# Performance work log

Measured on AMD Instinct MI355X. Metric: run time of the kernel, lower is better.

The kernel has to match this reference:

```python
import jax, jax.numpy as jnp
import numpy as np

B, N, IN, H, K, D, L = 8, 1024, 32, 32, 3, 16, 2  # batch, nodes, input_dim, hidden, cheb_k, embed_dim, layers


def setup_inputs() -> dict:
    key = jax.random.key(0)
    ks = jax.random.split(key, 4 + 4 * L)
    inp = {
        "xt": jax.random.normal(ks[0], (B, N, IN), jnp.float32),
        "init_state": jax.random.normal(ks[1], (L, B, N, H), jnp.float32),
        # row-normalized-ish support so the Chebyshev recursion stays bounded
        "support": jax.random.uniform(ks[2], (N, N), jnp.float32) / N,
        "embeddings": jax.random.normal(ks[3], (B, N, D), jnp.float32),
    }
    i = 4
    for l in range(L):
        cin = IN if l == 0 else H
        gi = K * (cin + H)
        inp[f"gate_w{l}"] = jax.random.normal(ks[i], (D, gi, 2 * H), jnp.float32) * (2.0 / (gi + 2 * H)) ** 0.5; i += 1
        inp[f"gate_b{l}"] = jax.random.normal(ks[i], (D, 2 * H), jnp.float32) * 0.05; i += 1
        inp[f"upd_w{l}"] = jax.random.normal(ks[i], (D, gi, H), jnp.float32) * (2.0 / (gi + H)) ** 0.5; i += 1
        inp[f"upd_b{l}"] = jax.random.normal(ks[i], (D, H), jnp.float32) * 0.05; i += 1
    return inp


def _cheb_gconv(x, support, emb, w_pool, b_pool):
    """HimGCN_share forward, meta_axis='ST', 2-D support.
    x: [B,N,C]; support: [N,N]; emb: [B,N,D];
    w_pool: [D, K*C, O]; b_pool: [D, O]. Returns [B,N,O]."""
    n = support.shape[0]
    graphs = [jnp.eye(n, dtype=x.dtype), support]
    for _ in range(2, K):
        graphs.append(2.0 * support @ graphs[-1] - graphs[-2])
    G = jnp.stack(graphs)                                   # [K,N,N]
    c = x.shape[-1]
    x_g = jnp.einsum('knm,bmc->bnkc', G, x).reshape(x.shape[0], n, K * c)  # concat over k
    # faithful to einsum('bni,bnio->bno') with bnio = einsum('bnd,dio->bnio'),
    # contracted in a memory-lighter order (same math)
    xe = jnp.einsum('bni,bnd->bnid', x_g, emb)              # [B,N,K*C,D]
    out = jnp.einsum('bnid,dio->bno', xe, w_pool)
    out = out + jnp.einsum('bnd,do->bno', emb, b_pool)
    return out


def _gcru_cell(x, state, support, emb, gw, gb, uw, ub):
    inp = jnp.concatenate([x, state], axis=-1)
    z_r = jax.nn.sigmoid(_cheb_gconv(inp, support, emb, gw, gb))
    z, r = z_r[..., :H], z_r[..., H:]
    cand = jnp.concatenate([x, z * state], axis=-1)
    hc = jnp.tanh(_cheb_gconv(cand, support, emb, uw, ub))
    return r * state + (1.0 - r) * hc


def reference(xt, init_state, support, embeddings,
              gate_w0, gate_b0, upd_w0, upd_b0,
              gate_w1, gate_b1, upd_w1, upd_b1):
    params = [(gate_w0, gate_b0, upd_w0, upd_b0), (gate_w1, gate_b1, upd_w1, upd_b1)]
    cur = xt
    hidden = []
    for l in range(L):
        gw, gb, uw, ub = params[l]
        cur = _gcru_cell(cur, init_state[l], support, embeddings, gw, gb, uw, ub)
        hidden.append(cur)
    return cur, jnp.stack(hidden)
```

## Files before the change

### kernel.cpp

```cpp
#include <hip/hip_runtime.h>
#include <math.h>

#define BB 8
#define NN 1024
#define HH 32
#define II 192
#define DD 16
#define BN (BB*NN)
#define FR 512

typedef __attribute__((ext_vector_type(8))) short short8v;
typedef __attribute__((ext_vector_type(4))) float float4v;

union Frag8 { short8v v; uint2 u[2]; uint4 q; };

static __device__ inline ushort bf(float x) {
  union { float f; unsigned u; } c; c.f = x;
  unsigned r = c.u + 0x7FFFu + ((c.u >> 16) & 1u);
  return (ushort)(r >> 16);
}

static __device__ inline uint4 pack8(const ushort e[8]) {
  uint4 v;
  v.x = (unsigned)e[0] | ((unsigned)e[1] << 16);
  v.y = (unsigned)e[2] | ((unsigned)e[3] << 16);
  v.z = (unsigned)e[4] | ((unsigned)e[5] << 16);
  v.w = (unsigned)e[6] | ((unsigned)e[7] << 16);
  return v;
}

template <int O>
static __device__ void prep_w_frag(const float* __restrict__ W,
                                   ushort* __restrict__ WF, int d,
                                   float* lds)
{
  constexpr int NCG = O / 16;
  const float* Wd = W + (size_t)d * II * O;
  ushort* WFd = WF + (size_t)d * NCG * 6 * FR;
  const int tid = threadIdx.x;
  for (int f = tid; f < II * O / 4; f += 256) {
    int i = f / (O / 4);
    int o4 = (f % (O / 4)) * 4;
    float4 v = *(const float4*)(Wd + (size_t)i * O + o4);
    lds[i * (O + 1) + o4 + 0] = v.x; lds[i * (O + 1) + o4 + 1] = v.y;
    lds[i * (O + 1) + o4 + 2] = v.z; lds[i * (O + 1) + o4 + 3] = v.w;
  }
  __syncthreads();
  for (int f = tid; f < NCG * 6 * 64; f += 256) {
    int rem = f % 384;
    int ks = rem >> 6, l = rem & 63;
    int o = (f / 384) * 16 + (l & 15);
    int kb = ks * 32 + (l >> 4) * 4;
    ushort e[8];
#pragma unroll
    for (int j = 0; j < 4; ++j) {
      e[j] = bf(lds[(kb + j) * (O + 1) + o]);
      e[4 + j] = bf(lds[(kb + 16 + j) * (O + 1) + o]);
    }
    *(uint4*)(WFd + (size_t)f * 8) = pack8(e);
  }
}

__global__ __launch_bounds__(256) void prep_all(
    const float* __restrict__ S,
    ushort* __restrict__ SbF, ushort* __restrict__ S2bF,
    const float* __restrict__ gw0, const float* __restrict__ gw1,
    ushort* __restrict__ wfg0, ushort* __restrict__ wfg1,
    const float* __restrict__ uw0, const float* __restrict__ uw1,
    ushort* __restrict__ wfu0, ushort* __restrict__ wfu1,
    const float* __restrict__ xt, const float* __restrict__ st0,
    const float* __restrict__ st1,
    ushort* __restrict__ xbTFg0, ushort* __restrict__ xbTFg1)
{
  union PrepSm {
    float wlds[II * 65];
    struct { ushort A[32][136]; ushort Bt[32][132]; ushort C2[32][36]; } s2;
    ushort T[32 * 72];
  };
  __shared__ PrepSm sm;
  int bx = blockIdx.x;
  const int tid = threadIdx.x;

  if (bx < 1024) {
    const int m0 = (bx >> 5) * 32, n0 = (bx & 31) * 32;
    const int w = tid >> 6, l = tid & 63;
    const int l15 = l & 15, l4 = l >> 4;
    const int wr = (w & 1) * 16, wc = (w >> 1) * 16;

    float4v acc = (float4v){0.f, 0.f, 0.f, 0.f};
    for (int k0 = 0; k0 < NN; k0 += 128) {
      __syncthreads();
#pragma unroll
      for (int q = 0; q < 2; ++q) {
        int f = tid + q * 256;
        int row = f >> 4, s8 = (f & 15) * 8;
        float4 lo = *(const float4*)(S + (size_t)(m0 + row) * NN + k0 + s8);
        float4 hi = *(const float4*)(S + (size_t)(m0 + row) * NN + k0 + s8 + 4);
        sm.s2.A[row][s8 + 0] = bf(lo.x); sm.s2.A[row][s8 + 1] = bf(lo.y);
        sm.s2.A[row][s8 + 2] = bf(lo.z); sm.s2.A[row][s8 + 3] = bf(lo.w);
        sm.s2.A[row][s8 + 4] = bf(hi.x); sm.s2.A[row][s8 + 5] = bf(hi.y);
        sm.s2.A[row][s8 + 6] = bf(hi.z); sm.s2.A[row][s8 + 7] = bf(hi.w);
      }
#pragma unroll
      for (int q = 0; q < 2; ++q) {
        int u = tid + q * 256;
        int kp = u >> 3, c4 = (u & 7) * 4;
        float4 a = *(const float4*)(S + (size_t)(k0 + 2 * kp) * NN + n0 + c4);
        float4 b = *(const float4*)(S + (size_t)(k0 + 2 * kp + 1) * NN + n0 + c4);
        *(unsigned*)&sm.s2.Bt[c4 + 0][2 * kp] = (unsigned)bf(a.x) | ((unsigned)bf(b.x) << 16);
        *(unsigned*)&sm.s2.Bt[c4 + 1][2 * kp] = (unsigned)bf(a.y) | ((unsigned)bf(b.y) << 16);
        *(unsigned*)&sm.s2.Bt[c4 + 2][2 * kp] = (unsigned)bf(a.z) | ((unsigned)bf(b.z) << 16);
        *(unsigned*)&sm.s2.Bt[c4 + 3][2 * kp] = (unsigned)bf(a.w) | ((unsigned)bf(b.w) << 16);
      }
      __syncthreads();
#pragma unroll
      for (int ks = 0; ks < 4; ++ks) {
        int kb = ks * 32 + l4 * 4;
        Frag8 af, bfr;
        af.u[0] = *(const uint2*)&sm.s2.A[wr + l15][kb];
        af.u[1] = *(const uint2*)&sm.s2.A[wr + l15][kb + 16];
        bfr.u[0] = *(const uint2*)&sm.s2.Bt[wc + l15][kb];
        bfr.u[1] = *(const uint2*)&sm.s2.Bt[wc + l15][kb + 16];
        acc = __builtin_amdgcn_mfma_f32_16x16x32_bf16(af.v, bfr.v, acc, 0, 0, 0);
      }
    }
    __syncthreads();
#pragma unroll
    for (int r = 0; r < 4; ++r)
      sm.s2.C2[wr + l4 * 4 + r][wc + l15] = bf(2.f * acc[r]);
    __syncthreads();
    if (tid < 128) {
      int fh = tid >> 6, l2 = tid & 63;
      ushort e[8];
#pragma unroll
      for (int j = 0; j < 4; ++j) {
        e[j] = sm.s2.C2[fh * 16 + (l2 & 15)][(l2 >> 4) * 4 + j];
        e[4 + j] = sm.s2.C2[fh * 16 + (l2 & 15)][(l2 >> 4) * 4 + 16 + j];
      }
      *(uint4*)(S2bF + ((size_t)((bx >> 5) * 2 + fh) * 32 + (bx & 31)) * FR +
                (size_t)l2 * 8) = pack8(e);
    }
    return;
  }
  bx -= 1024;
  if (bx < 32) {
    prep_w_frag<64>(bx >= 16 ? gw1 : gw0, bx >= 16 ? wfg1 : wfg0, bx & 15,
                    sm.wlds);
    return;
  }
  bx -= 32;
  if (bx < 32) {
    prep_w_frag<32>(bx >= 16 ? uw1 : uw0, bx >= 16 ? wfu1 : wfu0, bx & 15,
                    sm.wlds);
    return;
  }
  bx -= 32;
  if (bx < 384) {
    const int tensor = bx / 128, seg = bx % 128;
    const float* src = tensor == 0 ? xt : (tensor == 1 ? st0 : st1);
    ushort* T = sm.T;
    const int n0 = seg * 64;
#pragma unroll
    for (int q = 0; q < 2; ++q) {
      int f = tid + q * 256;
      int n = f >> 3, c4 = (f & 7) * 4;
      float4 v = *(const float4*)(src + (size_t)(n0 + n) * 32 + c4);
      T[(c4 + 0) * 72 + n] = bf(v.x); T[(c4 + 1) * 72 + n] = bf(v.y);
      T[(c4 + 2) * 72 + n] = bf(v.z); T[(c4 + 3) * 72 + n] = bf(v.w);
    }
    __syncthreads();
    {
      int gg = tid >> 7, ksl = (tid >> 6) & 1, l = tid & 63;
      int c = gg * 16 + (l & 15);
      int nb = ksl * 32 + (l >> 4) * 4;
      ushort e[8];
#pragma unroll
      for (int j = 0; j < 4; ++j) {
        e[j] = T[c * 72 + nb + j];
        e[4 + j] = T[c * 72 + nb + 16 + j];
      }
      int b = seg >> 4;
      int ks = (seg & 15) * 2 + ksl;
      ushort* dst; int g;
      if (tensor == 0)      { dst = xbTFg0; g = gg; }
      else if (tensor == 1) { dst = xbTFg0; g = 2 + gg; }
      else                  { dst = xbTFg1; g = 2 + gg; }
      *(uint4*)(dst + (((size_t)b * 4 + g) * 32 + ks) * FR + (size_t)l * 8) =
          pack8(e);
    }
    return;
  }
  bx -= 384;
  {
    const int mt = bx;
#pragma unroll
    for (int q = 0; q < 8; ++q) {
      int f = tid + q * 256;
      int ks = f >> 6, l = f & 63;
      int row = mt * 16 + (l & 15);
      int kb = ks * 32 + (l >> 4) * 4;
      float4 lo = *(const float4*)(S + (size_t)row * NN + kb);
      float4 hi = *(const float4*)(S + (size_t)row * NN + kb + 16);
      ushort e[8] = {bf(lo.x), bf(lo.y), bf(lo.z), bf(lo.w),
                     bf(hi.x), bf(hi.y), bf(hi.z), bf(hi.w)};
      *(uint4*)(SbF + ((size_t)mt * 32 + ks) * FR + (size_t)l * 8) = pack8(e);
    }
  }
}

template <int PHASE>
__global__ __launch_bounds__(512) void gconv_fused(
    const float* __restrict__ xb1,
    const float* __restrict__ xb2,
    const ushort* __restrict__ xbTF,
    const ushort* __restrict__ SbF,
    const ushort* __restrict__ S2bF,
    const float* __restrict__ emb,
    const ushort* __restrict__ WF,
    const float* __restrict__ bias,
    ushort* __restrict__ gT1c,
    float* __restrict__ gT2c,
    float* __restrict__ zr,
    float* __restrict__ zs,
    const float* __restrict__ state,
    float* __restrict__ hid,
    float* __restrict__ outp,
    ushort* __restrict__ xbTFout)
{
  constexpr int O = PHASE == 0 ? 64 : 32;
  constexpr int NCG = O / 16;
  __shared__ ushort A_sm[32][200];
  __shared__ float emb_sm[32][17];
  __shared__ float bias_sm[16][64];
  __shared__ float red1[4][2][64][4];
  __shared__ float red2[4][2][64][4];

  const int bid = blockIdx.x;
  const int mtp = (bid & 7) * 4 + ((bid >> 3) & 3);
  const int b = bid >> 5;
  const int m0 = mtp * 32;
  const int tid = threadIdx.x;
  const int w = tid >> 6, l = tid & 63;
  const int cw = w & 3, kh = w >> 2;
  const int l15 = l & 15, l4 = l >> 4;
  const int wcp = (PHASE == 0) ? cw * 16 : (cw & 1) * 16;

  if (tid < 128) {
    int row = tid >> 2, d4 = (tid & 3) * 4;
    float4 v = *(const float4*)(emb + ((size_t)b * NN + m0 + row) * DD + d4);
    emb_sm[row][d4 + 0] = v.x; emb_sm[row][d4 + 1] = v.y;
    emb_sm[row][d4 + 2] = v.z; emb_sm[row][d4 + 3] = v.w;
  }
  for (int f = tid; f < DD * O / 4; f += 512) {
    int d = f / (O / 4), o4 = (f % (O / 4)) * 4;
    *(float4*)&bias_sm[d][o4] = *(const float4*)(bias + (size_t)d * O + o4);
  }
  {
    int row = tid >> 4, c4 = (tid & 15) * 4;
    const float* src = (c4 < 32) ? xb1 : xb2;
    float4 v = *(const float4*)(src + ((size_t)b * NN + m0 + row) * 32 + (c4 & 31));
    ushort4 o; o.x = bf(v.x); o.y = bf(v.y); o.z = bf(v.z); o.w = bf(v.w);
    *(ushort4*)&A_sm[row][c4] = o;
  }
  if (PHASE == 1) {
#pragma unroll
    for (int q = 0; q < 2; ++q) {
      int e = tid + q * 512;
      int row = e >> 5, c = e & 31;
      size_t m = (size_t)b * NN + m0 + row;
      A_sm[row][64 + c] = gT1c[m * 32 + c];
      A_sm[row][128 + c] = bf(gT2c[m * 32 + c] - xb1[m * 32 + c]);
    }
  }

  float4v acc1[2], acc2[2];
#pragma unroll
  for (int rt = 0; rt < 2; ++rt) {
    acc1[rt] = (float4v){0.f, 0.f, 0.f, 0.f};
    acc2[rt] = (float4v){0.f, 0.f, 0.f, 0.f};
  }
  {
    const ushort* a1p0 = SbF + (size_t)(mtp * 2) * 32 * FR + (size_t)l * 8;
    const ushort* a2p0 = S2bF + (size_t)(mtp * 2) * 32 * FR + (size_t)l * 8;
    const ushort* bp = xbTF +
        (((size_t)b * NCG + (PHASE == 0 ? cw : (cw & 1))) * 32) * FR +
        (size_t)l * 8;
#pragma unroll 4
    for (int ks = kh * 16; ks < kh * 16 + 16; ++ks) {
      Frag8 a1r0, a1r1, a2r0, a2r1, b0;
      a1r0.q = *(const uint4*)(a1p0 + (size_t)ks * FR);
      a1r1.q = *(const uint4*)(a1p0 + (size_t)(32 + ks) * FR);
      a2r0.q = *(const uint4*)(a2p0 + (size_t)ks * FR);
      a2r1.q = *(const uint4*)(a2p0 + (size_t)(32 + ks) * FR);
      b0.q = *(const uint4*)(bp + (size_t)ks * FR);
      acc1[0] = __builtin_amdgcn_mfma_f32_16x16x32_bf16(a1r0.v, b0.v, acc1[0], 0, 0, 0);
      acc1[1] = __builtin_amdgcn_mfma_f32_16x16x32_bf16(a1r1.v, b0.v, acc1[1], 0, 0, 0);
      acc2[0] = __builtin_amdgcn_mfma_f32_16x16x32_bf16(a2r0.v, b0.v, acc2[0], 0, 0, 0);
      acc2[1] = __builtin_amdgcn_mfma_f32_16x16x32_bf16(a2r1.v, b0.v, acc2[1], 0, 0, 0);
    }
  }

  if (kh == 1) {
#pragma unroll
    for (int rt = 0; rt < 2; ++rt)
#pragma unroll
      for (int j = 0; j < 4; ++j) {
        red1[cw][rt][l][j] = acc1[rt][j];
        red2[cw][rt][l][j] = acc2[rt][j];
      }
  }
  __syncthreads();
  if (kh == 0) {
#pragma unroll
    for (int rt = 0; rt < 2; ++rt)
#pragma unroll
      for (int j = 0; j < 4; ++j) {
        acc1[rt][j] += red1[cw][rt][l][j];
        acc2[rt][j] += red2[cw][rt][l][j];
      }
    if (PHASE == 0 && cw < 2) {
#pragma unroll
      for (int rt = 0; rt < 2; ++rt)
#pragma unroll
        for (int r = 0; r < 4; ++r) {
          size_t m = (size_t)b * NN + m0 + rt * 16 + l4 * 4 + r;
          gT1c[m * 32 + wcp + l15] = bf(acc1[rt][r]);
          gT2c[m * 32 + wcp + l15] = acc2[rt][r];
        }
    }
    if (PHASE == 0 || cw < 2) {
      const int colX = (PHASE == 0 ? 0 : 32) + wcp + l15;
#pragma unroll
      for (int rt = 0; rt < 2; ++rt)
#pragma unroll
        for (int r = 0; r < 4; ++r) {
          int row = rt * 16 + l4 * 4 + r;
          const float* src = (colX < 32) ? xb1 : xb2;
          float xv = src[((size_t)b * NN + m0 + row) * 32 + (colX & 31)];
          A_sm[row][64 + colX] = bf(acc1[rt][r]);
          A_sm[row][128 + colX] = bf(acc2[rt][r] - xv);
        }
    }
  }
  __syncthreads();

  const int cg = (PHASE == 0) ? cw : (cw & 1);
  const int ocol = cg * 16 + l15;
  const int erow = l4 * 4;
  const ushort* wfp = WF + (size_t)cg * 6 * FR + (size_t)l * 8;

  float4v outacc[2];
  outacc[0] = (float4v){0.f, 0.f, 0.f, 0.f};
  outacc[1] = (float4v){0.f, 0.f, 0.f, 0.f};

#pragma unroll 2
  for (int d = kh * 8; d < kh * 8 + 8; ++d) {
    const ushort* wpd = wfp + (size_t)d * NCG * 6 * FR;
    float4v acc[2];
    acc[0] = (float4v){0.f, 0.f, 0.f, 0.f};
    acc[1] = (float4v){0.f, 0.f, 0.f, 0.f};
#pragma unroll
    for (int ks = 0; ks < 6; ++ks) {
      int kb = ks * 32 + l4 * 4;
      Frag8 af0, af1, bfr;
      af0.u[0] = *(const uint2*)&A_sm[l15][kb];
      af0.u[1] = *(const uint2*)&A_sm[l15][kb + 16];
      af1.u[0] = *(const uint2*)&A_sm[16 + l15][kb];
      af1.u[1] = *(const uint2*)&A_sm[16 + l15][kb + 16];
      bfr.q = *(const uint4*)(wpd + (size_t)ks * FR);
      acc[0] = __builtin_amdgcn_mfma_f32_16x16x32_bf16(af0.v, bfr.v, acc[0], 0, 0, 0);
      acc[1] = __builtin_amdgcn_mfma_f32_16x16x32_bf16(af1.v, bfr.v, acc[1], 0, 0, 0);
    }
    float bb = bias_sm[d][ocol];
#pragma unroll
    for (int rt = 0; rt < 2; ++rt) {
      outacc[rt][0] += emb_sm[rt * 16 + erow + 0][d] * (acc[rt][0] + bb);
      outacc[rt][1] += emb_sm[rt * 16 + erow + 1][d] * (acc[rt][1] + bb);
      outacc[rt][2] += emb_sm[rt * 16 + erow + 2][d] * (acc[rt][2] + bb);
      outacc[rt][3] += emb_sm[rt * 16 + erow + 3][d] * (acc[rt][3] + bb);
    }
  }

  if (kh == 1) {
#pragma unroll
    for (int rt = 0; rt < 2; ++rt)
#pragma unroll
      for (int j = 0; j < 4; ++j) red1[cw][rt][l][j] = outacc[rt][j];
  }
  __syncthreads();
  if (kh != 0) return;
#pragma unroll
  for (int rt = 0; rt < 2; ++rt)
#pragma unroll
    for (int j = 0; j < 4; ++j) outacc[rt][j] += red1[cw][rt][l][j];

  const int ksn = mtp;
  const int lanep = l4 * 16 + (ocol & 15);

  if (PHASE == 0) {
#pragma unroll
    for (int rt = 0; rt < 2; ++rt) {
      float zss[4];
#pragma unroll
      for (int r = 0; r < 4; ++r) {
        size_t m = (size_t)b * NN + m0 + rt * 16 + erow + r;
        float zv = 1.f / (1.f + __expf(-outacc[rt][r]));
        zr[m * 64 + ocol] = zv;
        if (ocol < 32) {
          float sv = zv * xb2[m * 32 + ocol];
          zs[m * 32 + ocol] = sv;
          zss[r] = sv;
        }
      }
      if (ocol < 32) {
        ushort4 pk; pk.x = bf(zss[0]); pk.y = bf(zss[1]);
        pk.z = bf(zss[2]); pk.w = bf(zss[3]);
        *(ushort4*)(xbTFout + (((size_t)b * 2 + (ocol >> 4)) * 32 + ksn) * FR +
                    (size_t)lanep * 8 + rt * 4) = pk;
      }
    }
  } else if (cw < 2) {
#pragma unroll
    for (int rt = 0; rt < 2; ++rt) {
      float res[4];
#pragma unroll
      for (int r = 0; r < 4; ++r) {
        size_t m = (size_t)b * NN + m0 + rt * 16 + erow + r;
        float hc = tanhf(outacc[rt][r]);
        float rg = zr[m * 64 + 32 + ocol];
        float st = state[m * 32 + ocol];
        res[r] = rg * st + (1.f - rg) * hc;
        hid[m * 32 + ocol] = res[r];
        if (outp) outp[m * 32 + ocol] = res[r];
      }
      if (xbTFout) {
        ushort4 pk; pk.x = bf(res[0]); pk.y = bf(res[1]);
        pk.z = bf(res[2]); pk.w = bf(res[3]);
        *(ushort4*)(xbTFout + (((size_t)b * 4 + (ocol >> 4)) * 32 + ksn) * FR +
                    (size_t)lanep * 8 + rt * 4) = pk;
      }
    }
  }
}

extern "C" void kernel_launch(void* const* d_in, const int* in_sizes, int n_in,
                              void* d_out, int out_size, void* d_ws, size_t ws_size,
                              hipStream_t stream)
{
  const float* xt         = (const float*)d_in[0];
  const float* init_state = (const float*)d_in[1];
  const float* S          = (const float*)d_in[2];
  const float* emb        = (const float*)d_in[3];

  float* out    = (float*)d_out;
  float* hidden = out + (size_t)BN * HH;

  float* zr   = (float*)d_ws;
  float* zs   = zr + (size_t)BN * 64;
  float* gT2c = zs + (size_t)BN * 32;
  ushort* gT1c = (ushort*)(gT2c + (size_t)BN * 32);
  ushort* SbF  = gT1c + (size_t)BN * 32;
  ushort* S2bF = SbF + (size_t)NN * NN;
  ushort* wfg0 = S2bF + (size_t)NN * NN;
  ushort* wfu0 = wfg0 + (size_t)DD * 4 * 6 * FR;
  ushort* wfg1 = wfu0 + (size_t)DD * 2 * 6 * FR;
  ushort* wfu1 = wfg1 + (size_t)DD * 4 * 6 * FR;
  ushort* xbTFg0 = wfu1 + (size_t)DD * 2 * 6 * FR;
  ushort* xbTFu0 = xbTFg0 + (size_t)BB * 4 * 32 * FR;
  ushort* xbTFg1 = xbTFu0 + (size_t)BB * 2 * 32 * FR;
  ushort* xbTFu1 = xbTFg1 + (size_t)BB * 4 * 32 * FR;

  const float* st0 = init_state;
  const float* st1 = init_state + (size_t)BN * HH;
  float* hid0 = hidden;
  float* hid1 = hidden + (size_t)BN * HH;

  prep_all<<<1536, 256, 0, stream>>>(
      S, SbF, S2bF,
      (const float*)d_in[4], (const float*)d_in[8], wfg0, wfg1,
      (const float*)d_in[6], (const float*)d_in[10], wfu0, wfu1,
      xt, st0, st1, xbTFg0, xbTFg1);

  gconv_fused<0><<<256, 512, 0, stream>>>(
      xt, st0, xbTFg0, SbF, S2bF, emb, wfg0, (const float*)d_in[5],
      gT1c, gT2c, zr, zs, nullptr, nullptr, nullptr, xbTFu0);
  gconv_fused<1><<<256, 512, 0, stream>>>(
      xt, zs, xbTFu0, SbF, S2bF, emb, wfu0, (const float*)d_in[7],
      gT1c, gT2c, zr, nullptr, st0, hid0, nullptr, xbTFg1);
  gconv_fused<0><<<256, 512, 0, stream>>>(
      hid0, st1, xbTFg1, SbF, S2bF, emb, wfg1, (const float*)d_in[9],
      gT1c, gT2c, zr, zs, nullptr, nullptr, nullptr, xbTFu1);
  gconv_fused<1><<<256, 512, 0, stream>>>(
      hid0, zs, xbTFu1, SbF, S2bF, emb, wfu1, (const float*)d_in[11],
      gT1c, gT2c, zr, nullptr, st1, hid1, out, nullptr);
}
```

Baseline: 91.22 us.

## Merge prep and four gconv launches into one cooperative kernel

Replaces the five separate kernel launches with one cooperative persistent kernel of 256 blocks x 512 threads. The prep jobs are distributed over the blocks in six rounds, and grid.sync() barriers separate the stages. The aim is to remove launch overhead and inter-kernel gaps. In exchange, half of each block's threads sit idle during prep, the prep work is serialized into rounds, and the kernel carries a larger shared memory union that may limit occupancy.

Measured after the change: 229.0 us. 151% more time.

```diff
diff --git a/kernel.cpp b/kernel.cpp
--- a/kernel.cpp
+++ b/kernel.cpp
@@ -1,5 +1,8 @@
 #include <hip/hip_runtime.h>
+#include <hip/hip_cooperative_groups.h>
 #include <math.h>
+
+namespace cg = cooperative_groups;
 
 #define BB 8
 #define NN 1024
@@ -28,6 +31,22 @@
   v.w = (unsigned)e[6] | ((unsigned)e[7] << 16);
   return v;
 }
+
+struct PrepSm {
+  union {
+    float wlds[II * 65];
+    struct { ushort A[32][136]; ushort Bt[32][132]; ushort C2[32][36]; } s2;
+    ushort T[32 * 72];
+  };
+};
+struct GconvSm {
+  ushort A_sm[32][200];
+  float emb_sm[32][17];
+  float bias_sm[16][64];
+  float red1[4][2][64][4];
+  float red2[4][2][64][4];
+};
+union MegaSm { PrepSm p; GconvSm g; };
 
 template <int O>
 static __device__ void prep_w_frag(const float* __restrict__ W,
@@ -38,30 +57,34 @@
   const float* Wd = W + (size_t)d * II * O;
   ushort* WFd = WF + (size_t)d * NCG * 6 * FR;
   const int tid = threadIdx.x;
-  for (int f = tid; f < II * O / 4; f += 256) {
-    int i = f / (O / 4);
-    int o4 = (f % (O / 4)) * 4;
-    float4 v = *(const float4*)(Wd + (size_t)i * O + o4);
-    lds[i * (O + 1) + o4 + 0] = v.x; lds[i * (O + 1) + o4 + 1] = v.y;
-    lds[i * (O + 1) + o4 + 2] = v.z; lds[i * (O + 1) + o4 + 3] = v.w;
+  if (tid < 256) {
+    for (int f = tid; f < II * O / 4; f += 256) {
+      int i = f / (O / 4);
+      int o4 = (f % (O / 4)) * 4;
+      float4 v = *(const float4*)(Wd + (size_t)i * O + o4);
+      lds[i * (O + 1) + o4 + 0] = v.x; lds[i * (O + 1) + o4 + 1] = v.y;
+      lds[i * (O + 1) + o4 + 2] = v.z; lds[i * (O + 1) + o4 + 3] = v.w;
+    }
   }
   __syncthreads();
-  for (int f = tid; f < NCG * 6 * 64; f += 256) {
-    int rem = f % 384;
-    int ks = rem >> 6, l = rem & 63;
-    int o = (f / 384) * 16 + (l & 15);
-    int kb = ks * 32 + (l >> 4) * 4;
-    ushort e[8];
-#pragma unroll
-    for (int j = 0; j < 4; ++j) {
-      e[j] = bf(lds[(kb + j) * (O + 1) + o]);
-      e[4 + j] = bf(lds[(kb + 16 + j) * (O + 1) + o]);
-    }
-    *(uint4*)(WFd + (size_t)f * 8) = pack8(e);
-  }
-}
-
-__global__ __launch_bounds__(256) void prep_all(
+  if (tid < 256) {
+    for (int f = tid; f < NCG * 6 * 64; f += 256) {
+      int rem = f % 384;
+      int ks = rem >> 6, l = rem & 63;
+      int o = (f / 384) * 16 + (l & 15);
+      int kb = ks * 32 + (l >> 4) * 4;
+      ushort e[8];
+#pragma unroll
+      for (int j = 0; j < 4; ++j) {
+        e[j] = bf(lds[(kb + j) * (O + 1) + o]);
+        e[4 + j] = bf(lds[(kb + 16 + j) * (O + 1) + o]);
+      }
+      *(uint4*)(WFd + (size_t)f * 8) = pack8(e);
+    }
+  }
+}
+
+static __device__ void prep_job(int bx, PrepSm& sm,
     const float* __restrict__ S,
     ushort* __restrict__ SbF, ushort* __restrict__ S2bF,
     const float* __restrict__ gw0, const float* __restrict__ gw1,
@@ -72,13 +95,6 @@
     const float* __restrict__ st1,
     ushort* __restrict__ xbTFg0, ushort* __restrict__ xbTFg1)
 {
-  union PrepSm {
-    float wlds[II * 65];
-    struct { ushort A[32][136]; ushort Bt[32][132]; ushort C2[32][36]; } s2;
-    ushort T[32 * 72];
-  };
-  __shared__ PrepSm sm;
-  int bx = blockIdx.x;
   const int tid = threadIdx.x;
 
   if (bx < 1024) {
@@ -90,44 +106,50 @@
     float4v acc = (float4v){0.f, 0.f, 0.f, 0.f};
     for (int k0 = 0; k0 < NN; k0 += 128) {
       __syncthreads();
-#pragma unroll
-      for (int q = 0; q < 2; ++q) {
-        int f = tid + q * 256;
-        int row = f >> 4, s8 = (f & 15) * 8;
-        float4 lo = *(const float4*)(S + (size_t)(m0 + row) * NN + k0 + s8);
-        float4 hi = *(const float4*)(S + (size_t)(m0 + row) * NN + k0 + s8 + 4);
-        sm.s2.A[row][s8 + 0] = bf(lo.x); sm.s2.A[row][s8 + 1] = bf(lo.y);
-        sm.s2.A[row][s8 + 2] = bf(lo.z); sm.s2.A[row][s8 + 3] = bf(lo.w);
-        sm.s2.A[row][s8 + 4] = bf(hi.x); sm.s2.A[row][s8 + 5] = bf(hi.y);
-        sm.s2.A[row][s8 + 6] = bf(hi.z); sm.s2.A[row][s8 + 7] = bf(hi.w);
-      }
-#pragma unroll
-      for (int q = 0; q < 2; ++q) {
-        int u = tid + q * 256;
-        int kp = u >> 3, c4 = (u & 7) * 4;
-        float4 a = *(const float4*)(S + (size_t)(k0 + 2 * kp) * NN + n0 + c4);
-        float4 b = *(const float4*)(S + (size_t)(k0 + 2 * kp + 1) * NN + n0 + c4);
-        *(unsigned*)&sm.s2.Bt[c4 + 0][2 * kp] = (unsigned)bf(a.x) | ((unsigned)bf(b.x) << 16);
-        *(unsigned*)&sm.s2.Bt[c4 + 1][2 * kp] = (unsigned)bf(a.y) | ((unsigned)bf(b.y) << 16);
-        *(unsigned*)&sm.s2.Bt[c4 + 2][2 * kp] = (unsigned)bf(a.z) | ((unsigned)bf(b.z) << 16);
-        *(unsigned*)&sm.s2.Bt[c4 + 3][2 * kp] = (unsigned)bf(a.w) | ((unsigned)bf(b.w) << 16);
+      if (tid < 256) {
+#pragma unroll
+        for (int q = 0; q < 2; ++q) {
+          int f = tid + q * 256;
+          int row = f >> 4, s8 = (f & 15) * 8;
+          float4 lo = *(const float4*)(S + (size_t)(m0 + row) * NN + k0 + s8);
+          float4 hi = *(const float4*)(S + (size_t)(m0 + row) * NN + k0 + s8 + 4);
+          sm.s2.A[row][s8 + 0] = bf(lo.x); sm.s2.A[row][s8 + 1] = bf(lo.y);
+          sm.s2.A[row][s8 + 2] = bf(lo.z); sm.s2.A[row][s8 + 3] = bf(lo.w);
+          sm.s2.A[row][s8 + 4] = bf(hi.x); sm.s2.A[row][s8 + 5] = bf(hi.y);
+          sm.s2.A[row][s8 + 6] = bf(hi.z); sm.s2.A[row][s8 + 7] = bf(hi.w);
+        }
+#pragma unroll
+        for (int q = 0; q < 2; ++q) {
+          int u = tid + q * 256;
+          int kp = u >> 3, c4 = (u & 7) * 4;
+          float4 a = *(const float4*)(S + (size_t)(k0 + 2 * kp) * NN + n0 + c4);
+          float4 b = *(const float4*)(S + (size_t)(k0 + 2 * kp + 1) * NN + n0 + c4);
+          *(unsigned*)&sm.s2.Bt[c4 + 0][2 * kp] = (unsigned)bf(a.x) | ((unsigned)bf(b.x) << 16);
+          *(unsigned*)&sm.s2.Bt[c4 + 1][2 * kp] = (unsigned)bf(a.y) | ((unsigned)bf(b.y) << 16);
+          *(unsigned*)&sm.s2.Bt[c4 + 2][2 * kp] = (unsigned)bf(a.z) | ((unsigned)bf(b.z) << 16);
+          *(unsigned*)&sm.s2.Bt[c4 + 3][2 * kp] = (unsigned)bf(a.w) | ((unsigned)bf(b.w) << 16);
+        }
       }
       __syncthreads();
-#pragma unroll
-      for (int ks = 0; ks < 4; ++ks) {
-        int kb = ks * 32 + l4 * 4;
-        Frag8 af, bfr;
-        af.u[0] = *(const uint2*)&sm.s2.A[wr + l15][kb];
-        af.u[1] = *(const uint2*)&sm.s2.A[wr + l15][kb + 16];
-        bfr.u[0] = *(const uint2*)&sm.s2.Bt[wc + l15][kb];
-        bfr.u[1] = *(const uint2*)&sm.s2.Bt[wc + l15][kb + 16];
-        acc = __builtin_amdgcn_mfma_f32_16x16x32_bf16(af.v, bfr.v, acc, 0, 0, 0);
+      if (tid < 256) {
+#pragma unroll
+        for (int ks = 0; ks < 4; ++ks) {
+          int kb = ks * 32 + l4 * 4;
+          Frag8 af, bfr;
+          af.u[0] = *(const uint2*)&sm.s2.A[wr + l15][kb];
+          af.u[1] = *(const uint2*)&sm.s2.A[wr + l15][kb + 16];
+          bfr.u[0] = *(const uint2*)&sm.s2.Bt[wc + l15][kb];
+          bfr.u[1] = *(const uint2*)&sm.s2.Bt[wc + l15][kb + 16];
+          acc = __builtin_amdgcn_mfma_f32_16x16x32_bf16(af.v, bfr.v, acc, 0, 0, 0);
+        }
       }
     }
     __syncthreads();
-#pragma unroll
-    for (int r = 0; r < 4; ++r)
-      sm.s2.C2[wr + l4 * 4 + r][wc + l15] = bf(2.f * acc[r]);
+    if (tid < 256) {
+#pragma unroll
+      for (int r = 0; r < 4; ++r)
+        sm.s2.C2[wr + l4 * 4 + r][wc + l15] = bf(2.f * acc[r]);
+    }
     __syncthreads();
     if (tid < 128) {
       int fh = tid >> 6, l2 = tid & 63;
@@ -160,16 +182,18 @@
     const float* src = tensor == 0 ? xt : (tensor == 1 ? st0 : st1);
     ushort* T = sm.T;
     const int n0 = seg * 64;
-#pragma unroll
-    for (int q = 0; q < 2; ++q) {
-      int f = tid + q * 256;
-      int n = f >> 3, c4 = (f & 7) * 4;
-      float4 v = *(const float4*)(src + (size_t)(n0 + n) * 32 + c4);
-      T[(c4 + 0) * 72 + n] = bf(v.x); T[(c4 + 1) * 72 + n] = bf(v.y);
-      T[(c4 + 2) * 72 + n] = bf(v.z); T[(c4 + 3) * 72 + n] = bf(v.w);
+    if (tid < 256) {
+#pragma unroll
+      for (int q = 0; q < 2; ++q) {
+        int f = tid + q * 256;
+        int n = f >> 3, c4 = (f & 7) * 4;
+        float4 v = *(const float4*)(src + (size_t)(n0 + n) * 32 + c4);
+        T[(c4 + 0) * 72 + n] = bf(v.x); T[(c4 + 1) * 72 + n] = bf(v.y);
+        T[(c4 + 2) * 72 + n] = bf(v.z); T[(c4 + 3) * 72 + n] = bf(v.w);
+      }
     }
     __syncthreads();
-    {
+    if (tid < 256) {
       int gg = tid >> 7, ksl = (tid >> 6) & 1, l = tid & 63;
       int c = gg * 16 + (l & 15);
       int nb = ksl * 32 + (l >> 4) * 4;
@@ -193,47 +217,38 @@
   bx -= 384;
   {
     const int mt = bx;
-#pragma unroll
-    for (int q = 0; q < 8; ++q) {
-      int f = tid + q * 256;
-      int ks = f >> 6, l = f & 63;
-      int row = mt * 16 + (l & 15);
-      int kb = ks * 32 + (l >> 4) * 4;
-      float4 lo = *(const float4*)(S + (size_t)row * NN + kb);
-      float4 hi = *(const float4*)(S + (size_t)row * NN + kb + 16);
-      ushort e[8] = {bf(lo.x), bf(lo.y), bf(lo.z), bf(lo.w),
-                     bf(hi.x), bf(hi.y), bf(hi.z), bf(hi.w)};
-      *(uint4*)(SbF + ((size_t)mt * 32 + ks) * FR + (size_t)l * 8) = pack8(e);
+    if (tid < 256) {
+#pragma unroll
+      for (int q = 0; q < 8; ++q) {
+        int f = tid + q * 256;
+        int ks = f >> 6, l = f & 63;
+        int row = mt * 16 + (l & 15);
+        int kb = ks * 32 + (l >> 4) * 4;
+        float4 lo = *(const float4*)(S + (size_t)row * NN + kb);
+        float4 hi = *(const float4*)(S + (size_t)row * NN + kb + 16);
+        ushort e[8] = {bf(lo.x), bf(lo.y), bf(lo.z), bf(lo.w),
+                       bf(hi.x), bf(hi.y), bf(hi.z), bf(hi.w)};
+        *(uint4*)(SbF + ((size_t)mt * 32 + ks) * FR + (size_t)l * 8) = pack8(e);
+      }
     }
   }
 }
 
 template <int PHASE>
-__global__ __launch_bounds__(512) void gconv_fused(
-    const float* __restrict__ xb1,
-    const float* __restrict__ xb2,
+static __device__ void gconv_body(GconvSm& sm,
+    const float* __restrict__ xb1, const float* __restrict__ xb2,
     const ushort* __restrict__ xbTF,
-    const ushort* __restrict__ SbF,
-    const ushort* __restrict__ S2bF,
+    const ushort* __restrict__ SbF, const ushort* __restrict__ S2bF,
     const float* __restrict__ emb,
-    const ushort* __restrict__ WF,
-    const float* __restrict__ bias,
-    ushort* __restrict__ gT1c,
-    float* __restrict__ gT2c,
-    float* __restrict__ zr,
-    float* __restrict__ zs,
+    const ushort* __restrict__ WF, const float* __restrict__ bias,
+    ushort* __restrict__ gT1c, float* __restrict__ gT2c,
+    float* __restrict__ zr, float* __restrict__ zs,
     const float* __restrict__ state,
-    float* __restrict__ hid,
-    float* __restrict__ outp,
+    float* __restrict__ hid, float* __restrict__ outp,
     ushort* __restrict__ xbTFout)
 {
   constexpr int O = PHASE == 0 ? 64 : 32;
   constexpr int NCG = O / 16;
-  __shared__ ushort A_sm[32][200];
-  __shared__ float emb_sm[32][17];
-  __shared__ float bias_sm[16][64];
-  __shared__ float red1[4][2][64][4];
-  __shared__ float red2[4][2][64][4];
 
   const int bid = blockIdx.x;
   const int mtp = (bid & 7) * 4 + ((bid >> 3) & 3);
@@ -248,19 +263,19 @@
   if (tid < 128) {
     int row = tid >> 2, d4 = (tid & 3) * 4;
     float4 v = *(const float4*)(emb + ((size_t)b * NN + m0 + row) * DD + d4);
-    emb_sm[row][d4 + 0] = v.x; emb_sm[row][d4 + 1] = v.y;
-    emb_sm[row][d4 + 2] = v.z; emb_sm[row][d4 + 3] = v.w;
+    sm.emb_sm[row][d4 + 0] = v.x; sm.emb_sm[row][d4 + 1] = v.y;
+    sm.emb_sm[row][d4 + 2] = v.z; sm.emb_sm[row][d4 + 3] = v.w;
   }
   for (int f = tid; f < DD * O / 4; f += 512) {
     int d = f / (O / 4), o4 = (f % (O / 4)) * 4;
-    *(float4*)&bias_sm[d][o4] = *(const float4*)(bias + (size_t)d * O + o4);
+    *(float4*)&sm.bias_sm[d][o4] = *(const float4*)(bias + (size_t)d * O + o4);
   }
   {
     int row = tid >> 4, c4 = (tid & 15) * 4;
     const float* src = (c4 < 32) ? xb1 : xb2;
     float4 v = *(const float4*)(src + ((size_t)b * NN + m0 + row) * 32 + (c4 & 31));
     ushort4 o; o.x = bf(v.x); o.y = bf(v.y); o.z = bf(v.z); o.w = bf(v.w);
-    *(ushort4*)&A_sm[row][c4] = o;
+    *(ushort4*)&sm.A_sm[row][c4] = o;
   }
   if (PHASE == 1) {
 #pragma unroll
@@ -268,8 +283,8 @@
       int e = tid + q * 512;
       int row = e >> 5, c = e & 31;
       size_t m = (size_t)b * NN + m0 + row;
-      A_sm[row][64 + c] = gT1c[m * 32 + c];
-      A_sm[row][128 + c] = bf(gT2c[m * 32 + c] - xb1[m * 32 + c]);
+      sm.A_sm[row][64 + c] = gT1c[m * 32 + c];
+      sm.A_sm[row][128 + c] = bf(gT2c[m * 32 + c] - xb1[m * 32 + c]);
     }
   }
 
@@ -305,8 +320,8 @@
     for (int rt = 0; rt < 2; ++rt)
 #pragma unroll
       for (int j = 0; j < 4; ++j) {
-        red1[cw][rt][l][j] = acc1[rt][j];
-        red2[cw][rt][l][j] = acc2[rt][j];
+        sm.red1[cw][rt][l][j] = acc1[rt][j];
+        sm.red2[cw][rt][l][j] = acc2[rt][j];
       }
   }
   __syncthreads();
@@ -315,8 +330,8 @@
     for (int rt = 0; rt < 2; ++rt)
 #pragma unroll
       for (int j = 0; j < 4; ++j) {
-        acc1[rt][j] += red1[cw][rt][l][j];
-        acc2[rt][j] += red2[cw][rt][l][j];
+        acc1[rt][j] += sm.red1[cw][rt][l][j];
+        acc2[rt][j] += sm.red2[cw][rt][l][j];
       }
     if (PHASE == 0 && cw < 2) {
 #pragma unroll
@@ -337,8 +352,8 @@
           int row = rt * 16 + l4 * 4 + r;
           const float* src = (colX < 32) ? xb1 : xb2;
           float xv = src[((size_t)b * NN + m0 + row) * 32 + (colX & 31)];
-          A_sm[row][64 + colX] = bf(acc1[rt][r]);
-          A_sm[row][128 + colX] = bf(acc2[rt][r] - xv);
+          sm.A_sm[row][64 + colX] = bf(acc1[rt][r]);
+          sm.A_sm[row][128 + colX] = bf(acc2[rt][r] - xv);
         }
     }
   }
@@ -363,21 +378,21 @@
     for (int ks = 0; ks < 6; ++ks) {
       int kb = ks * 32 + l4 * 4;
       Frag8 af0, af1, bfr;
-      af0.u[0] = *(const uint2*)&A_sm[l15][kb];
-      af0.u[1] = *(const uint2*)&A_sm[l15][kb + 16];
-      af1.u[0] = *(const uint2*)&A_sm[16 + l15][kb];
-      af1.u[1] = *(const uint2*)&A_sm[16 + l15][kb + 16];
+      af0.u[0] = *(const uint2*)&sm.A_sm[l15][kb];
+      af0.u[1] = *(const uint2*)&sm.A_sm[l15][kb + 16];
+      af1.u[0] = *(const uint2*)&sm.A_sm[16 + l15][kb];
+      af1.u[1] = *(const uint2*)&sm.A_sm[16 + l15][kb + 16];
       bfr.q = *(const uint4*)(wpd + (size_t)ks * FR);
       acc[0] = __builtin_amdgcn_mfma_f32_16x16x32_bf16(af0.v, bfr.v, acc[0], 0, 0, 0);
       acc[1] = __builtin_amdgcn_mfma_f32_16x16x32_bf16(af1.v, bfr.v, acc[1], 0, 0, 0);
     }
-    float bb = bias_sm[d][ocol];
+    float bb = sm.bias_sm[d][ocol];
 #pragma unroll
     for (int rt = 0; rt < 2; ++rt) {
-      outacc[rt][0] += emb_sm[rt * 16 + erow + 0][d] * (acc[rt][0] + bb);
-      outacc[rt][1] += emb_sm[rt * 16 + erow + 1][d] * (acc[rt][1] + bb);
-      outacc[rt][2] += emb_sm[rt * 16 + erow + 2][d] * (acc[rt][2] + bb);
-      outacc[rt][3] += emb_sm[rt * 16 + erow + 3][d] * (acc[rt][3] + bb);
+      outacc[rt][0] += sm.emb_sm[rt * 16 + erow + 0][d] * (acc[rt][0] + bb);
+      outacc[rt][1] += sm.emb_sm[rt * 16 + erow + 1][d] * (acc[rt][1] + bb);
+      outacc[rt][2] += sm.emb_sm[rt * 16 + erow + 2][d] * (acc[rt][2] + bb);
+      outacc[rt][3] += sm.emb_sm[rt * 16 + erow + 3][d] * (acc[rt][3] + bb);
     }
   }
 
@@ -385,14 +400,14 @@
 #pragma unroll
     for (int rt = 0; rt < 2; ++rt)
 #pragma unroll
-      for (int j = 0; j < 4; ++j) red1[cw][rt][l][j] = outacc[rt][j];
+      for (int j = 0; j < 4; ++j) sm.red1[cw][rt][l][j] = outacc[rt][j];
   }
   __syncthreads();
   if (kh != 0) return;
 #pragma unroll
   for (int rt = 0; rt < 2; ++rt)
 #pragma unroll
-    for (int j = 0; j < 4; ++j) outacc[rt][j] += red1[cw][rt][l][j];
+    for (int j = 0; j < 4; ++j) outacc[rt][j] += sm.red1[cw][rt][l][j];
 
   const int ksn = mtp;
   const int lanep = l4 * 16 + (ocol & 15);
@@ -443,19 +458,16 @@
   }
 }
 
-extern "C" void kernel_launch(void* const* d_in, const int* in_sizes, int n_in,
-                              void* d_out, int out_size, void* d_ws, size_t ws_size,
-                              hipStream_t stream)
+__global__ __launch_bounds__(512) void mega(
+    const float* xt, const float* init_state, const float* S, const float* emb,
+    const float* gw0, const float* gb0, const float* uw0, const float* ub0,
+    const float* gw1, const float* gb1, const float* uw1, const float* ub1,
+    float* out, void* ws)
 {
-  const float* xt         = (const float*)d_in[0];
-  const float* init_state = (const float*)d_in[1];
-  const float* S          = (const float*)d_in[2];
-  const float* emb        = (const float*)d_in[3];
-
-  float* out    = (float*)d_out;
-  float* hidden = out + (size_t)BN * HH;
-
-  float* zr   = (float*)d_ws;
+  __shared__ MegaSm sm;
+  cg::grid_group grid = cg::this_grid();
+
+  float* zr   = (float*)ws;
   float* zs   = zr + (size_t)BN * 64;
   float* gT2c = zs + (size_t)BN * 32;
   ushort* gT1c = (ushort*)(gT2c + (size_t)BN * 32);
@@ -470,27 +482,57 @@
   ushort* xbTFg1 = xbTFu0 + (size_t)BB * 2 * 32 * FR;
   ushort* xbTFu1 = xbTFg1 + (size_t)BB * 4 * 32 * FR;
 
+  float* hidden = out + (size_t)BN * HH;
   const float* st0 = init_state;
   const float* st1 = init_state + (size_t)BN * HH;
   float* hid0 = hidden;
   float* hid1 = hidden + (size_t)BN * HH;
 
-  prep_all<<<1536, 256, 0, stream>>>(
-      S, SbF, S2bF,
-      (const float*)d_in[4], (const float*)d_in[8], wfg0, wfg1,
-      (const float*)d_in[6], (const float*)d_in[10], wfu0, wfu1,
-      xt, st0, st1, xbTFg0, xbTFg1);
-
-  gconv_fused<0><<<256, 512, 0, stream>>>(
-      xt, st0, xbTFg0, SbF, S2bF, emb, wfg0, (const float*)d_in[5],
-      gT1c, gT2c, zr, zs, nullptr, nullptr, nullptr, xbTFu0);
-  gconv_fused<1><<<256, 512, 0, stream>>>(
-      xt, zs, xbTFu0, SbF, S2bF, emb, wfu0, (const float*)d_in[7],
-      gT1c, gT2c, zr, nullptr, st0, hid0, nullptr, xbTFg1);
-  gconv_fused<0><<<256, 512, 0, stream>>>(
-      hid0, st1, xbTFg1, SbF, S2bF, emb, wfg1, (const float*)d_in[9],
-      gT1c, gT2c, zr, zs, nullptr, nullptr, nullptr, xbTFu1);
-  gconv_fused<1><<<256, 512, 0, stream>>>(
-      hid0, zs, xbTFu1, SbF, S2bF, emb, wfu1, (const float*)d_in[11],
-      gT1c, gT2c, zr, nullptr, st1, hid1, out, nullptr);
-}
+#pragma unroll 1
+  for (int j = 0; j < 6; ++j) {
+    prep_job(blockIdx.x + j * 256, sm.p, S, SbF, S2bF,
+             gw0, gw1, wfg0, wfg1, uw0, uw1, wfu0, wfu1,
+             xt, st0, st1, xbTFg0, xbTFg1);
+    __syncthreads();
+  }
+  grid.sync();
+
+  gconv_body<0>(sm.g, xt, st0, xbTFg0, SbF, S2bF, emb, wfg0, gb0,
+                gT1c, gT2c, zr, zs, nullptr, nullptr, nullptr, xbTFu0);
+  grid.sync();
+  gconv_body<1>(sm.g, xt, zs, xbTFu0, SbF, S2bF, emb, wfu0, ub0,
+                gT1c, gT2c, zr, nullptr, st0, hid0, nullptr, xbTFg1);
+  grid.sync();
+  gconv_body<0>(sm.g, hid0, st1, xbTFg1, SbF, S2bF, emb, wfg1, gb1,
+                gT1c, gT2c, zr, zs, nullptr, nullptr, nullptr, xbTFu1);
+  grid.sync();
+  gconv_body<1>(sm.g, hid0, zs, xbTFu1, SbF, S2bF, emb, wfu1, ub1,
+                gT1c, gT2c, zr, nullptr, st1, hid1, out, nullptr);
+}
+
+extern "C" void kernel_launch(void* const* d_in, const int* in_sizes, int n_in,
+                              void* d_out, int out_size, void* d_ws, size_t ws_size,
+                              hipStream_t stream)
+{
+  const float* xt         = (const float*)d_in[0];
+  const float* init_state = (const float*)d_in[1];
+  const float* S          = (const float*)d_in[2];
+  const float* emb        = (const float*)d_in[3];
+  const float* gw0 = (const float*)d_in[4];
+  const float* gb0 = (const float*)d_in[5];
+  const float* uw0 = (const float*)d_in[6];
+  const float* ub0 = (const float*)d_in[7];
+  const float* gw1 = (const float*)d_in[8];
+  const float* gb1 = (const float*)d_in[9];
+  const float* uw1 = (const float*)d_in[10];
+  const float* ub1 = (const float*)d_in[11];
+  float* out = (float*)d_out;
+  void* ws = d_ws;
+
+  void* args[] = {&xt, &init_state, &S, &emb,
+                  &gw0, &gb0, &uw0, &ub0,
+                  &gw1, &gb1, &uw1, &ub1,
+                  &out, &ws};
+  hipLaunchCooperativeKernel((const void*)mega, dim3(256), dim3(512),
+                             args, 0, stream);
+}
```
